# Optimization experiments

Measured on AMD Instinct MI355X. Metric: run time of the kernel, lower is better.

The kernel has to match this reference:

```python
import jax, jax.numpy as jnp
import numpy as np

N, E, IN, HID, OUT = 50000, 800000, 128, 64, 32
ALPHA, BETA, DIVIDER = 0.5, 0.5, 5.0


def _gcn_conv(x, edge_index, W, b, alpha=ALPHA, beta=BETA):
    """DirectedGCNConv.forward: add self loops, linear, degree-normalized gather-mul-scatter."""
    n = x.shape[0]
    loops = jnp.arange(n, dtype=edge_index.dtype)
    row = jnp.concatenate([edge_index[0], loops])  # sources
    col = jnp.concatenate([edge_index[1], loops])  # targets
    x = x @ W.T + b                                # [n, out]
    ones = jnp.ones(row.shape[0], dtype=x.dtype)
    in_deg = jax.ops.segment_sum(ones, col, num_segments=n)
    out_deg = jax.ops.segment_sum(ones, row, num_segments=n)
    norm = in_deg[col] ** (-alpha) * out_deg[row] ** (-beta)  # [E+n]
    msgs = norm[:, None] * x[row]                  # gather + scale
    return jax.ops.segment_sum(msgs, col, num_segments=n)  # scatter-add aggr


def _source_enc(x, ei, W1, b1, W2, b2):
    x = jax.nn.relu(_gcn_conv(x, ei, W1, b1))
    return _gcn_conv(x, jnp.flip(ei, axis=0), W2, b2)


def _target_enc(x, ei, W1, b1, W2, b2):
    x = jax.nn.relu(_gcn_conv(x, jnp.flip(ei, axis=0), W1, b1))
    return _gcn_conv(x, ei, W2, b2)


def setup_inputs() -> dict:
    key = jax.random.key(0)
    ks = jax.random.split(key, 24)

    def lin(kw, kb, o, i, scale):
        return (jax.random.normal(kw, (o, i), jnp.float32) * scale,
                jax.random.normal(kb, (o,), jnp.float32) * 0.01)

    s1 = (2.0 / (IN + HID)) ** 0.5
    s2 = (2.0 / (HID + OUT)) ** 0.5
    inp = {
        "s": jax.random.normal(ks[0], (N, IN), jnp.float32),
        "t": jax.random.normal(ks[1], (N, IN), jnp.float32),
        "edge_index": jax.random.randint(ks[2], (2, E), 0, N, jnp.int32),
        "noise_s": jax.random.normal(ks[3], (N, OUT), jnp.float32),
        "noise_t": jax.random.normal(ks[4], (N, OUT), jnp.float32),
    }
    names = ["sm", "sl", "tm", "tl"]  # source/target mu/logstd encoders
    k = 5
    for nm in names:
        W1, b1 = lin(ks[k], ks[k + 1], HID, IN, s1); k += 2
        W2, b2 = lin(ks[k], ks[k + 1], OUT, HID, s2); k += 2
        inp[nm + "1_W"], inp[nm + "1_b"] = W1, b1
        inp[nm + "2_W"], inp[nm + "2_b"] = W2, b2
    return inp


def reference(s, t, edge_index, noise_s, noise_t,
              sm1_W, sm1_b, sm2_W, sm2_b,
              sl1_W, sl1_b, sl2_W, sl2_b,
              tm1_W, tm1_b, tm2_W, tm2_b,
              tl1_W, tl1_b, tl2_W, tl2_b):
    s_mu = _source_enc(s, edge_index, sm1_W, sm1_b, sm2_W, sm2_b)
    s_logstd = _source_enc(s, edge_index, sl1_W, sl1_b, sl2_W, sl2_b)
    t_mu = _target_enc(t, edge_index, tm1_W, tm1_b, tm2_W, tm2_b)
    t_logstd = _target_enc(t, edge_index, tl1_W, tl1_b, tl2_W, tl2_b)
    # reparametrize_edges (training mode), noise materialized as input
    s_out = s_mu + noise_s * jnp.exp(s_logstd) / DIVIDER
    t_out = t_mu + noise_t * jnp.exp(t_logstd) / DIVIDER
    return (s_out, t_out)
```

## Files before the change

kernel.cpp:

```cpp
#include <hip/hip_runtime.h>
#include <hip/hip_fp16.h>
#include <math.h>

#define N_NODES 50000
#define NPACK 25000
#define E_EDGES 800000
#define NCHUNKS ((N_NODES + 1023) / 1024)
#define LIN_BLOCKS 1564
#define QCH 64
#define CHUNK (E_EDGES / QCH)
#define CHUNK4 (CHUNK / 4)
#define OCT_NODES 6250
#define OCT_PACK 3125
#define HF_BLOCKS 1024
#define FILL_GRID (HF_BLOCKS + LIN_BLOCKS)

typedef _Float16 half8 __attribute__((ext_vector_type(8)));
typedef float f32x4 __attribute__((ext_vector_type(4)));

__device__ inline float fac_from(unsigned int u) {
    unsigned short us = (unsigned short)(u >> 16);
    __half h;
    __builtin_memcpy(&h, &us, 2);
    return __half2float(h);
}

__device__ inline int unpack_cnt(const unsigned int* cntp, int i) {
    unsigned int w = cntp[i >> 1];
    return (i & 1) ? (int)(w >> 16) : (int)(w & 0xffff);
}

__device__ inline uint4 nt_load4(const uint4* p) {
    const unsigned long long* q = (const unsigned long long*)p;
    unsigned long long a = __builtin_nontemporal_load(q);
    unsigned long long b = __builtin_nontemporal_load(q + 1);
    uint4 r;
    r.x = (unsigned int)a; r.y = (unsigned int)(a >> 32);
    r.z = (unsigned int)b; r.w = (unsigned int)(b >> 32);
    return r;
}

__global__ __launch_bounds__(256) void hist_kernel(const int* __restrict__ ei0,
                                                   const int* __restrict__ ei1,
                                                   unsigned int* __restrict__ ghist) {
    __shared__ unsigned int h[OCT_PACK];
    int bx = blockIdx.x;
    int oct = bx & 7, q = (bx >> 3) & 63, dir = bx >> 9;
    int tid = threadIdx.x;
    for (int i = tid; i < OCT_PACK; i += 256) h[i] = 0;
    __syncthreads();
    const int* key = dir ? ei0 : ei1;
    const uint4* key4 = (const uint4*)(key + q * CHUNK);
    int lo = oct * OCT_NODES;
    for (int j = tid; j < CHUNK4; j += 256) {
        uint4 k4 = nt_load4(key4 + j);
        int vv[4] = { (int)k4.x, (int)k4.y, (int)k4.z, (int)k4.w };
#pragma unroll
        for (int e = 0; e < 4; ++e) {
            unsigned int d = (unsigned int)(vv[e] - lo);
            if (d < OCT_NODES) atomicAdd(&h[d >> 1], 1u << ((d & 1) * 16));
        }
    }
    __syncthreads();
    unsigned int* g = ghist + (size_t)(dir * QCH + q) * NPACK + oct * OCT_PACK;
    for (int i = tid; i < OCT_PACK; i += 256) g[i] = h[i];
}

__global__ __launch_bounds__(256) void nodescan_kernel(unsigned int* __restrict__ ghist,
                                                       unsigned int* __restrict__ cntp) {
    int vp = blockIdx.x * 256 + threadIdx.x;
    int dir = blockIdx.y;
    if (vp >= NPACK) return;
    unsigned int lo = 0, hi = 0;
    unsigned int* g = ghist + (size_t)dir * QCH * NPACK + vp;
#pragma unroll 4
    for (int q = 0; q < QCH; ++q) {
        unsigned int w = g[(size_t)q * NPACK];
        g[(size_t)q * NPACK] = lo | (hi << 16);
        lo += w & 0xffff;
        hi += w >> 16;
    }
    cntp[dir * NPACK + vp] = lo | (hi << 16);
}

__global__ __launch_bounds__(1024) void scan_chunk2_kernel(const unsigned int* __restrict__ cntp,
                                                           int* __restrict__ offs_f,
                                                           int* __restrict__ offs_b,
                                                           int* __restrict__ part_f,
                                                           int* __restrict__ part_b, int n) {
    const unsigned int* cnt = cntp + (blockIdx.y ? NPACK : 0);
    int* offs = blockIdx.y ? offs_b : offs_f;
    int* partials = blockIdx.y ? part_b : part_f;
    __shared__ int sh[1024];
    int tid = threadIdx.x;
    int i = blockIdx.x * 1024 + tid;
    int v = (i < n) ? unpack_cnt(cnt, i) : 0;
    sh[tid] = v;
    __syncthreads();
    for (int off = 1; off < 1024; off <<= 1) {
        int add = (tid >= off) ? sh[tid - off] : 0;
        __syncthreads();
        sh[tid] += add;
        __syncthreads();
    }
    if (i < n) offs[i] = sh[tid] - v;
    if (tid == 1023) partials[blockIdx.x] = sh[tid];
}

__global__ __launch_bounds__(64) void scan_partials2_kernel(int* part_f, int* part_b, int nchunks) {
    int* p = blockIdx.x ? part_b : part_f;
    __shared__ int sh[64];
    int tid = threadIdx.x;
    int v = (tid < nchunks) ? p[tid] : 0;
    sh[tid] = v;
    __syncthreads();
    for (int off = 1; off < 64; off <<= 1) {
        int add = (tid >= off) ? sh[tid - off] : 0;
        __syncthreads();
        sh[tid] += add;
        __syncthreads();
    }
    if (tid < nchunks) p[tid] = sh[tid] - v;
    if (tid == 63) p[nchunks] = sh[63];
}

__global__ __launch_bounds__(256) void addback_deg_kernel(int* __restrict__ offs_f,
                                                          int* __restrict__ offs_b,
                                                          const int* __restrict__ part_f,
                                                          const int* __restrict__ part_b,
                                                          const unsigned int* __restrict__ cntp,
                                                          float* dsi, float* dti,
                                                          unsigned short* __restrict__ h_dsi,
                                                          unsigned short* __restrict__ h_dti,
                                                          int n, int nchunks) {
    int i = blockIdx.x * 256 + threadIdx.x;
    if (blockIdx.y == 0) {
        if (i < n) {
            offs_f[i] += part_f[i >> 10];
            float f = rsqrtf((float)(unpack_cnt(cntp, i) + 1));
            dti[i] = f;
            __half hf = __float2half(f);
            unsigned short hb; __builtin_memcpy(&hb, &hf, 2);
            h_dti[i] = hb;
        } else if (i == n) offs_f[n] = part_f[nchunks];
    } else {
        if (i < n) {
            offs_b[i] += part_b[i >> 10];
            float f = rsqrtf((float)(unpack_cnt(cntp + NPACK, i) + 1));
            dsi[i] = f;
            __half hf = __float2half(f);
            unsigned short hb; __builtin_memcpy(&hb, &hf, 2);
            h_dsi[i] = hb;
        } else if (i == n) offs_b[n] = part_b[nchunks];
    }
}

__global__ __launch_bounds__(256) void fill_lin1_kernel(const int* __restrict__ ei0,
                                                        const int* __restrict__ ei1,
                                                        const unsigned int* __restrict__ ghist,
                                                        const int* __restrict__ offs_f,
                                                        const int* __restrict__ offs_b,
                                                        const unsigned short* __restrict__ h_dsi,
                                                        const unsigned short* __restrict__ h_dti,
                                                        unsigned int* __restrict__ pay_f,
                                                        unsigned int* __restrict__ pay_b,
                                                        const float* __restrict__ Xs,
                                                        const float* __restrict__ Xt,
                                                        const float* __restrict__ sWa,
                                                        const float* __restrict__ sba,
                                                        const float* __restrict__ sWb,
                                                        const float* __restrict__ sbb,
                                                        const float* __restrict__ tWa,
                                                        const float* __restrict__ tba,
                                                        const float* __restrict__ tWb,
                                                        const float* __restrict__ tbb,
                                                        __half* __restrict__ As,
                                                        __half* __restrict__ At, int n) {
    __shared__ unsigned int h[OCT_PACK];
    __shared__ unsigned int pref_sh[OCT_PACK];
    int bx = blockIdx.x;
    int tid = threadIdx.x;
    if (bx < HF_BLOCKS) {
        int oct = bx & 7, q = (bx >> 3) & 63, dir = bx >> 9;
        const unsigned int* pref = ghist + (size_t)(dir * QCH + q) * NPACK + oct * OCT_PACK;
        for (int i = tid; i < OCT_PACK; i += 256) {
            h[i] = 0;
            pref_sh[i] = __builtin_nontemporal_load(pref + i);
        }
        __syncthreads();
        const int* key = dir ? ei0 : ei1;
        const int* pid = dir ? ei1 : ei0;
        const unsigned short* hfac = dir ? h_dti : h_dsi;
        const int* offs = dir ? offs_b : offs_f;
        unsigned int* pay = dir ? pay_b : pay_f;
        const uint4* key4 = (const uint4*)(key + q * CHUNK);
        const uint4* pid4 = (const uint4*)(pid + q * CHUNK);
        int lo = oct * OCT_NODES;
        for (int j = tid; j < CHUNK4; j += 256) {
            uint4 k4 = nt_load4(key4 + j);
            uint4 p4 = nt_load4(pid4 + j);
            int vv[4] = { (int)k4.x, (int)k4.y, (int)k4.z, (int)k4.w };
            int pp[4] = { (int)p4.x, (int)p4.y, (int)p4.z, (int)p4.w };
#pragma unroll
            for (int e = 0; e < 4; ++e) {
                int v = vv[e];
                unsigned int d = (unsigned int)(v - lo);
                if (d < OCT_NODES) {
                    int sh = (d & 1) * 16;
                    unsigned int old = atomicAdd(&h[d >> 1], 1u << sh);
                    int rank = (int)((old >> sh) & 0xffff);
                    int cb = (int)((pref_sh[d >> 1] >> sh) & 0xffff);
                    int id = pp[e];
                    unsigned int hb = hfac[id];
                    pay[offs[v] + cb + rank] = (unsigned int)id | (hb << 16);
                }
            }
        }
        return;
    }
    int lidx = bx - HF_BLOCKS;
    int y = lidx & 1;
    int xb = lidx >> 1;
    const float* X = y ? Xt : Xs;
    const float* Wset[2] = { y ? tWa : sWa, y ? tWb : sWb };
    const float* bset[2] = { y ? tba : sba, y ? tbb : sbb };
    __half* A = y ? At : As;

    int w = tid >> 6, lane = tid & 63;
    int quad = lane >> 4, col = lane & 15;
    int node0 = xb * 64 + w * 16;

    half8 afrag[4];
    {
        int row = node0 + col;
        if (row >= n) row = n - 1;
        const float* xr = X + (size_t)row * 128 + quad * 8;
#pragma unroll
        for (int kc = 0; kc < 4; ++kc) {
            float4 f0 = *(const float4*)(xr + kc * 32);
            float4 f1 = *(const float4*)(xr + kc * 32 + 4);
            half8 hh;
            hh[0] = (_Float16)f0.x; hh[1] = (_Float16)f0.y;
            hh[2] = (_Float16)f0.z; hh[3] = (_Float16)f0.w;
            hh[4] = (_Float16)f1.x; hh[5] = (_Float16)f1.y;
            hh[6] = (_Float16)f1.z; hh[7] = (_Float16)f1.w;
            afrag[kc] = hh;
        }
    }

#pragma unroll
    for (int set = 0; set < 2; ++set) {
        const float* Ws = Wset[set];
#pragma unroll
        for (int nt = 0; nt < 4; ++nt) {
            float bb = bset[set][nt * 16 + col];
            f32x4 acc = { bb, bb, bb, bb };
            const float* wr = Ws + (size_t)(nt * 16 + col) * 128 + quad * 8;
#pragma unroll
            for (int kc = 0; kc < 4; ++kc) {
                float4 f0 = *(const float4*)(wr + kc * 32);
                float4 f1 = *(const float4*)(wr + kc * 32 + 4);
                half8 bfr;
                bfr[0] = (_Float16)f0.x; bfr[1] = (_Float16)f0.y;
                bfr[2] = (_Float16)f0.z; bfr[3] = (_Float16)f0.w;
                bfr[4] = (_Float16)f1.x; bfr[5] = (_Float16)f1.y;
                bfr[6] = (_Float16)f1.z; bfr[7] = (_Float16)f1.w;
                acc = __builtin_amdgcn_mfma_f32_16x16x32_f16(afrag[kc], bfr, acc, 0, 0, 0);
            }
#pragma unroll
            for (int r = 0; r < 4; ++r) {
                int node = node0 + quad * 4 + r;
                if (node < n)
                    A[(size_t)node * 128 + set * 64 + nt * 16 + col] = __float2half(acc[r]);
            }
        }
    }
}

__device__ inline void acc_fma(float* acc, uint4 u, float f) {
    const __half2* h = (const __half2*)&u;
    float2 f0 = __half22float2(h[0]);
    float2 f1 = __half22float2(h[1]);
    float2 f2 = __half22float2(h[2]);
    float2 f3 = __half22float2(h[3]);
    acc[0] += f * f0.x; acc[1] += f * f0.y; acc[2] += f * f1.x; acc[3] += f * f1.y;
    acc[4] += f * f2.x; acc[5] += f * f2.y; acc[6] += f * f3.x; acc[7] += f * f3.y;
}

__global__ __launch_bounds__(256) void pull_lin2_kernel(const __half* __restrict__ As,
                                                        const __half* __restrict__ At,
                                                        __half* __restrict__ Cs,
                                                        __half* __restrict__ Ct,
                                                        const int* __restrict__ offs_f,
                                                        const int* __restrict__ offs_b,
                                                        const unsigned int* __restrict__ pay_f,
                                                        const unsigned int* __restrict__ pay_b,
                                                        const float* __restrict__ dsi,
                                                        const float* __restrict__ dti,
                                                        const float* __restrict__ sW2a,
                                                        const float* __restrict__ sb2a,
                                                        const float* __restrict__ sW2b,
                                                        const float* __restrict__ sb2b,
                                                        const float* __restrict__ tW2a,
                                                        const float* __restrict__ tb2a,
                                                        const float* __restrict__ tW2b,
                                                        const float* __restrict__ tb2b, int n) {
    int y = blockIdx.y;
    const __half* xw = y ? At : As;
    __half* C = y ? Ct : Cs;
    const int* offs = y ? offs_b : offs_f;
    const unsigned int* pay = y ? pay_b : pay_f;
    const float* fac_self  = y ? dsi : dti;
    const float* fac_other = y ? dti : dsi;
    const float* W2a = y ? tW2a : sW2a;  const float* b2a = y ? tb2a : sb2a;
    const float* W2b = y ? tW2b : sW2b;  const float* b2b = y ? tb2b : sb2b;

    __shared__ float Wt[64 * 66];
    __shared__ float bsh[64];
    __shared__ float xs[16 * 132];

    int tid = threadIdx.x;
    for (int idx = tid; idx < 2048; idx += 256) {
        int o = idx >> 6, k = idx & 63;
        Wt[k * 66 + o]      = W2a[idx];
        Wt[k * 66 + 33 + o] = W2b[idx];
    }
    if (tid < 32) { bsh[tid] = b2a[tid]; bsh[32 + tid] = b2b[tid]; }

    int ln = tid >> 4;
    int f4 = tid & 15;
    int v = blockIdx.x * 16 + ln;
    int i = offs[v], end = offs[v + 1];
    const uint4* xw16 = (const uint4*)xw;

    float acc[8] = {0, 0, 0, 0, 0, 0, 0, 0};
    acc_fma(acc, xw16[v * 16 + f4], fac_other[v]);
    while (i < end && (i & 3)) {
        unsigned int pk = pay[i];
        acc_fma(acc, xw16[(pk & 0xffff) * 16 + f4], fac_from(pk));
        ++i;
    }
    for (; i + 3 < end; i += 4) {
        uint4 pk = *(const uint4*)(pay + i);
        int s0 = pk.x & 0xffff, s1 = pk.y & 0xffff;
        int s2 = pk.z & 0xffff, s3 = pk.w & 0xffff;
        uint4 ua = xw16[s0 * 16 + f4];
        uint4 ub = xw16[s1 * 16 + f4];
        uint4 uc = xw16[s2 * 16 + f4];
        uint4 ud = xw16[s3 * 16 + f4];
        acc_fma(acc, ua, fac_from(pk.x));
        acc_fma(acc, ub, fac_from(pk.y));
        acc_fma(acc, uc, fac_from(pk.z));
        acc_fma(acc, ud, fac_from(pk.w));
    }
    for (; i < end; ++i) {
        unsigned int pk = pay[i];
        acc_fma(acc, xw16[(pk & 0xffff) * 16 + f4], fac_from(pk));
    }

    float fs = fac_self[v];
    float4 a0, a1;
    a0.x = fmaxf(acc[0] * fs, 0.0f); a0.y = fmaxf(acc[1] * fs, 0.0f);
    a0.z = fmaxf(acc[2] * fs, 0.0f); a0.w = fmaxf(acc[3] * fs, 0.0f);
    a1.x = fmaxf(acc[4] * fs, 0.0f); a1.y = fmaxf(acc[5] * fs, 0.0f);
    a1.z = fmaxf(acc[6] * fs, 0.0f); a1.w = fmaxf(acc[7] * fs, 0.0f);
    *(float4*)&xs[ln * 132 + f4 * 8]     = a0;
    *(float4*)&xs[ln * 132 + f4 * 8 + 4] = a1;
    __syncthreads();

    int nn = tid >> 5, o = tid & 31;
    const float* x0 = &xs[nn * 132];
    const float* x1 = &xs[(nn + 8) * 132];
    float am0 = bsh[o], al0 = bsh[32 + o];
    float am1 = am0,    al1 = al0;
#pragma unroll 4
    for (int k = 0; k < 64; ++k) {
        float wm = Wt[k * 66 + o], wl = Wt[k * 66 + 33 + o];
        am0 += x0[k] * wm;  al0 += x0[64 + k] * wl;
        am1 += x1[k] * wm;  al1 += x1[64 + k] * wl;
    }
    int v0 = blockIdx.x * 16 + nn;
    int v1 = v0 + 8;
    C[v0 * 64 + o]      = __float2half(am0);
    C[v0 * 64 + 32 + o] = __float2half(al0);
    C[v1 * 64 + o]      = __float2half(am1);
    C[v1 * 64 + 32 + o] = __float2half(al1);
}

__global__ __launch_bounds__(256) void final_pull2_kernel(const __half* __restrict__ Cs,
                                                          const __half* __restrict__ Ct,
                                                          float* __restrict__ out_s,
                                                          float* __restrict__ out_t,
                                                          const int* __restrict__ offs_f,
                                                          const int* __restrict__ offs_b,
                                                          const unsigned int* __restrict__ pay_f,
                                                          const unsigned int* __restrict__ pay_b,
                                                          const float* __restrict__ dsi,
                                                          const float* __restrict__ dti,
                                                          const float* __restrict__ noise_s,
                                                          const float* __restrict__ noise_t,
                                                          int n) {
    int y = blockIdx.y;
    const __half* xw = y ? Ct : Cs;
    float* out = y ? out_t : out_s;
    const int* offs = y ? offs_f : offs_b;
    const unsigned int* pay = y ? pay_f : pay_b;
    const float* fac_self  = y ? dti : dsi;
    const float* fac_other = y ? dsi : dti;
    const float* noise = y ? noise_t : noise_s;

    const uint4* xw16 = (const uint4*)xw;
    int ln = threadIdx.x >> 3;
    int f4 = threadIdx.x & 7;
    int v = blockIdx.x * 32 + ln;
    if (v >= n) return;
    int i = offs[v], end = offs[v + 1];

    float acc[8] = {0, 0, 0, 0, 0, 0, 0, 0};
    acc_fma(acc, xw16[v * 8 + f4], fac_other[v]);
    while (i < end && (i & 3)) {
        unsigned int pk = pay[i];
        acc_fma(acc, xw16[(pk & 0xffff) * 8 + f4], fac_from(pk));
        ++i;
    }
    for (; i + 3 < end; i += 4) {
        uint4 pk = *(const uint4*)(pay + i);
        int s0 = pk.x & 0xffff, s1 = pk.y & 0xffff;
        int s2 = pk.z & 0xffff, s3 = pk.w & 0xffff;
        uint4 ua = xw16[s0 * 8 + f4];
        uint4 ub = xw16[s1 * 8 + f4];
        uint4 uc = xw16[s2 * 8 + f4];
        uint4 ud = xw16[s3 * 8 + f4];
        acc_fma(acc, ua, fac_from(pk.x));
        acc_fma(acc, ub, fac_from(pk.y));
        acc_fma(acc, uc, fac_from(pk.z));
        acc_fma(acc, ud, fac_from(pk.w));
    }
    for (; i < end; ++i) {
        unsigned int pk = pay[i];
        acc_fma(acc, xw16[(pk & 0xffff) * 8 + f4], fac_from(pk));
    }

    float fs = fac_self[v];
#pragma unroll
    for (int j = 0; j < 8; ++j) acc[j] *= fs;

    int lane = threadIdx.x & 63;
    float lg[8];
#pragma unroll
    for (int j = 0; j < 8; ++j) lg[j] = __shfl(acc[j], lane + 4);
    if (f4 < 4) {
        const float4* nz4 = (const float4*)noise;
        float4 n0 = nz4[v * 8 + f4 * 2];
        float4 n1 = nz4[v * 8 + f4 * 2 + 1];
        float4 r0, r1;
        r0.x = acc[0] + n0.x * expf(lg[0]) * 0.2f;
        r0.y = acc[1] + n0.y * expf(lg[1]) * 0.2f;
        r0.z = acc[2] + n0.z * expf(lg[2]) * 0.2f;
        r0.w = acc[3] + n0.w * expf(lg[3]) * 0.2f;
        r1.x = acc[4] + n1.x * expf(lg[4]) * 0.2f;
        r1.y = acc[5] + n1.y * expf(lg[5]) * 0.2f;
        r1.z = acc[6] + n1.z * expf(lg[6]) * 0.2f;
        r1.w = acc[7] + n1.w * expf(lg[7]) * 0.2f;
        float4* o4 = (float4*)out;
        o4[v * 8 + f4 * 2]     = r0;
        o4[v * 8 + f4 * 2 + 1] = r1;
    }
}

extern "C" void kernel_launch(void* const* d_in, const int* in_sizes, int n_in,
                              void* d_out, int out_size, void* d_ws, size_t ws_size,
                              hipStream_t stream) {
    const float* s       = (const float*)d_in[0];
    const float* t       = (const float*)d_in[1];
    const int*   ei      = (const int*)d_in[2];
    const float* noise_s = (const float*)d_in[3];
    const float* noise_t = (const float*)d_in[4];
    const float* sm1_W = (const float*)d_in[5];  const float* sm1_b = (const float*)d_in[6];
    const float* sm2_W = (const float*)d_in[7];  const float* sm2_b = (const float*)d_in[8];
    const float* sl1_W = (const float*)d_in[9];  const float* sl1_b = (const float*)d_in[10];
    const float* sl2_W = (const float*)d_in[11]; const float* sl2_b = (const float*)d_in[12];
    const float* tm1_W = (const float*)d_in[13]; const float* tm1_b = (const float*)d_in[14];
    const float* tm2_W = (const float*)d_in[15]; const float* tm2_b = (const float*)d_in[16];
    const float* tl1_W = (const float*)d_in[17]; const float* tl1_b = (const float*)d_in[18];
    const float* tl2_W = (const float*)d_in[19]; const float* tl2_b = (const float*)d_in[20];

    const int* ei0 = ei;
    const int* ei1 = ei + E_EDGES;

    __half* A_s = (__half*)d_ws;
    __half* A_t = A_s + (size_t)N_NODES * 128;
    __half* C_s = A_t + (size_t)N_NODES * 128;
    __half* C_t = C_s + (size_t)N_NODES * 64;
    unsigned int* pay_fwd = (unsigned int*)(C_t + (size_t)N_NODES * 64);
    unsigned int* pay_bwd = pay_fwd + E_EDGES;
    float* dsi = (float*)(pay_bwd + E_EDGES);
    float* dti = dsi + N_NODES;
    int* offs_fwd = (int*)(dti + N_NODES);
    int* offs_bwd = offs_fwd + N_NODES + 1;
    unsigned int* cntp = (unsigned int*)(offs_bwd + N_NODES + 1);
    int* part_fwd = (int*)(cntp + 2 * NPACK);
    int* part_bwd = part_fwd + NCHUNKS + 1;
    unsigned short* h_dsi = (unsigned short*)(part_bwd + NCHUNKS + 1);
    unsigned short* h_dti = h_dsi + N_NODES;

    unsigned int* ghist = (unsigned int*)C_s;

    float* s_out = (float*)d_out;
    float* t_out = (float*)d_out + N_NODES * 32;

    dim3 blk(256);
    dim3 agrid((N_NODES + 1 + 255) / 256, 2);
    dim3 pgrid(N_NODES / 16, 2);
    dim3 fgrid((N_NODES + 31) / 32, 2);
    dim3 nsgrid((NPACK + 255) / 256, 2);

    hist_kernel<<<HF_BLOCKS, blk, 0, stream>>>(ei0, ei1, ghist);
    nodescan_kernel<<<nsgrid, blk, 0, stream>>>(ghist, cntp);
    scan_chunk2_kernel<<<dim3(NCHUNKS, 2), 1024, 0, stream>>>(
        cntp, offs_fwd, offs_bwd, part_fwd, part_bwd, N_NODES);
    scan_partials2_kernel<<<2, 64, 0, stream>>>(part_fwd, part_bwd, NCHUNKS);
    addback_deg_kernel<<<agrid, blk, 0, stream>>>(offs_fwd, offs_bwd, part_fwd, part_bwd,
                                                  cntp, dsi, dti, h_dsi, h_dti,
                                                  N_NODES, NCHUNKS);
    fill_lin1_kernel<<<FILL_GRID, blk, 0, stream>>>(
        ei0, ei1, ghist, offs_fwd, offs_bwd, h_dsi, h_dti, pay_fwd, pay_bwd,
        s, t, sm1_W, sm1_b, sl1_W, sl1_b, tm1_W, tm1_b, tl1_W, tl1_b,
        A_s, A_t, N_NODES);

    pull_lin2_kernel<<<pgrid, blk, 0, stream>>>(A_s, A_t, C_s, C_t,
                                                offs_fwd, offs_bwd, pay_fwd, pay_bwd,
                                                dsi, dti,
                                                sm2_W, sm2_b, sl2_W, sl2_b,
                                                tm2_W, tm2_b, tl2_W, tl2_b, N_NODES);
    final_pull2_kernel<<<fgrid, blk, 0, stream>>>(C_s, C_t, s_out, t_out,
                                                  offs_fwd, offs_bwd, pay_fwd, pay_bwd,
                                                  dsi, dti, noise_s, noise_t, N_NODES);
}
```

Before: 369.2 us.

## Record per-bucket edge lists in histogram pass; fill only listed edges

The histogram pass now also writes, for each (direction, chunk, node-range) bucket, a compact list of edge indices that fall in that range, using wave ballot plus a shared counter. The fill kernel then reads only those listed edges, instead of rescanning the whole key chunk in all eight range blocks. Output positions come from per-node shared cursors built from prefix offsets. The first linear layer moves from the fill kernel into the histogram kernel's extra blocks. The lists are capped at a fixed capacity, so a bucket that overflows would silently drop edges, and edge order within a node becomes nondeterministic.

```diff
diff --git a/kernel.cpp b/kernel.cpp
--- a/kernel.cpp
+++ b/kernel.cpp
@@ -13,7 +13,8 @@
 #define OCT_NODES 6250
 #define OCT_PACK 3125
 #define HF_BLOCKS 1024
-#define FILL_GRID (HF_BLOCKS + LIN_BLOCKS)
+#define HL_GRID (HF_BLOCKS + LIN_BLOCKS)
+#define LCAP 2048
 
 typedef _Float16 half8 __attribute__((ext_vector_type(8)));
 typedef float f32x4 __attribute__((ext_vector_type(4)));
@@ -30,40 +31,121 @@
     return (i & 1) ? (int)(w >> 16) : (int)(w & 0xffff);
 }
 
-__device__ inline uint4 nt_load4(const uint4* p) {
-    const unsigned long long* q = (const unsigned long long*)p;
-    unsigned long long a = __builtin_nontemporal_load(q);
-    unsigned long long b = __builtin_nontemporal_load(q + 1);
-    uint4 r;
-    r.x = (unsigned int)a; r.y = (unsigned int)(a >> 32);
-    r.z = (unsigned int)b; r.w = (unsigned int)(b >> 32);
-    return r;
-}
-
-__global__ __launch_bounds__(256) void hist_kernel(const int* __restrict__ ei0,
-                                                   const int* __restrict__ ei1,
-                                                   unsigned int* __restrict__ ghist) {
+__global__ __launch_bounds__(256) void hist_lin1_kernel(const int* __restrict__ ei0,
+                                                        const int* __restrict__ ei1,
+                                                        unsigned int* __restrict__ ghist,
+                                                        unsigned short* __restrict__ list,
+                                                        unsigned int* __restrict__ cnt_bkt,
+                                                        const float* __restrict__ Xs,
+                                                        const float* __restrict__ Xt,
+                                                        const float* __restrict__ sWa,
+                                                        const float* __restrict__ sba,
+                                                        const float* __restrict__ sWb,
+                                                        const float* __restrict__ sbb,
+                                                        const float* __restrict__ tWa,
+                                                        const float* __restrict__ tba,
+                                                        const float* __restrict__ tWb,
+                                                        const float* __restrict__ tbb,
+                                                        __half* __restrict__ As,
+                                                        __half* __restrict__ At, int n) {
     __shared__ unsigned int h[OCT_PACK];
+    __shared__ unsigned int lcnt;
     int bx = blockIdx.x;
-    int oct = bx & 7, q = (bx >> 3) & 63, dir = bx >> 9;
     int tid = threadIdx.x;
-    for (int i = tid; i < OCT_PACK; i += 256) h[i] = 0;
-    __syncthreads();
-    const int* key = dir ? ei0 : ei1;
-    const uint4* key4 = (const uint4*)(key + q * CHUNK);
-    int lo = oct * OCT_NODES;
-    for (int j = tid; j < CHUNK4; j += 256) {
-        uint4 k4 = nt_load4(key4 + j);
-        int vv[4] = { (int)k4.x, (int)k4.y, (int)k4.z, (int)k4.w };
-#pragma unroll
-        for (int e = 0; e < 4; ++e) {
-            unsigned int d = (unsigned int)(vv[e] - lo);
-            if (d < OCT_NODES) atomicAdd(&h[d >> 1], 1u << ((d & 1) * 16));
+    if (bx < HF_BLOCKS) {
+        int oct = bx & 7, q = (bx >> 3) & 63, dir = bx >> 9;
+        for (int i = tid; i < OCT_PACK; i += 256) h[i] = 0;
+        if (tid == 0) lcnt = 0;
+        __syncthreads();
+        const int* key = dir ? ei0 : ei1;
+        const uint4* key4 = (const uint4*)(key + q * CHUNK);
+        unsigned short* lst = list + ((size_t)(dir * QCH + q) * 8 + oct) * LCAP;
+        int lo = oct * OCT_NODES;
+        int lane = tid & 63;
+        for (int j = tid; j < CHUNK4; j += 256) {
+            uint4 k4 = key4[j];
+            int vv[4] = { (int)k4.x, (int)k4.y, (int)k4.z, (int)k4.w };
+#pragma unroll
+            for (int e = 0; e < 4; ++e) {
+                unsigned int d = (unsigned int)(vv[e] - lo);
+                bool pred = d < OCT_NODES;
+                if (pred) atomicAdd(&h[d >> 1], 1u << ((d & 1) * 16));
+                unsigned long long m = __ballot(pred);
+                if (m) {
+                    int pre = __popcll(m & ((1ull << lane) - 1));
+                    int tot = __popcll(m);
+                    int ldr = __ffsll((unsigned long long)m) - 1;
+                    unsigned int base = 0;
+                    if (lane == ldr) base = atomicAdd(&lcnt, (unsigned int)tot);
+                    base = __shfl(base, ldr);
+                    unsigned int slot = base + (unsigned int)pre;
+                    if (pred && slot < LCAP) lst[slot] = (unsigned short)(j * 4 + e);
+                }
+            }
         }
-    }
-    __syncthreads();
-    unsigned int* g = ghist + (size_t)(dir * QCH + q) * NPACK + oct * OCT_PACK;
-    for (int i = tid; i < OCT_PACK; i += 256) g[i] = h[i];
+        __syncthreads();
+        unsigned int* g = ghist + (size_t)(dir * QCH + q) * NPACK + oct * OCT_PACK;
+        for (int i = tid; i < OCT_PACK; i += 256) g[i] = h[i];
+        if (tid == 0) cnt_bkt[dir * 512 + q * 8 + oct] = (lcnt < LCAP) ? lcnt : LCAP;
+        return;
+    }
+    int lidx = bx - HF_BLOCKS;
+    int y = lidx & 1;
+    int xb = lidx >> 1;
+    const float* X = y ? Xt : Xs;
+    const float* Wset[2] = { y ? tWa : sWa, y ? tWb : sWb };
+    const float* bset[2] = { y ? tba : sba, y ? tbb : sbb };
+    __half* A = y ? At : As;
+
+    int w = tid >> 6, lane = tid & 63;
+    int quad = lane >> 4, col = lane & 15;
+    int node0 = xb * 64 + w * 16;
+
+    half8 afrag[4];
+    {
+        int row = node0 + col;
+        if (row >= n) row = n - 1;
+        const float* xr = X + (size_t)row * 128 + quad * 8;
+#pragma unroll
+        for (int kc = 0; kc < 4; ++kc) {
+            float4 f0 = *(const float4*)(xr + kc * 32);
+            float4 f1 = *(const float4*)(xr + kc * 32 + 4);
+            half8 hh;
+            hh[0] = (_Float16)f0.x; hh[1] = (_Float16)f0.y;
+            hh[2] = (_Float16)f0.z; hh[3] = (_Float16)f0.w;
+            hh[4] = (_Float16)f1.x; hh[5] = (_Float16)f1.y;
+            hh[6] = (_Float16)f1.z; hh[7] = (_Float16)f1.w;
+            afrag[kc] = hh;
+        }
+    }
+
+#pragma unroll
+    for (int set = 0; set < 2; ++set) {
+        const float* Ws = Wset[set];
+#pragma unroll
+        for (int nt = 0; nt < 4; ++nt) {
+            float bb = bset[set][nt * 16 + col];
+            f32x4 acc = { bb, bb, bb, bb };
+            const float* wr = Ws + (size_t)(nt * 16 + col) * 128 + quad * 8;
+#pragma unroll
+            for (int kc = 0; kc < 4; ++kc) {
+                float4 f0 = *(const float4*)(wr + kc * 32);
+                float4 f1 = *(const float4*)(wr + kc * 32 + 4);
+                half8 bfr;
+                bfr[0] = (_Float16)f0.x; bfr[1] = (_Float16)f0.y;
+                bfr[2] = (_Float16)f0.z; bfr[3] = (_Float16)f0.w;
+                bfr[4] = (_Float16)f1.x; bfr[5] = (_Float16)f1.y;
+                bfr[6] = (_Float16)f1.z; bfr[7] = (_Float16)f1.w;
+                acc = __builtin_amdgcn_mfma_f32_16x16x32_f16(afrag[kc], bfr, acc, 0, 0, 0);
+            }
+#pragma unroll
+            for (int r = 0; r < 4; ++r) {
+                int node = node0 + quad * 4 + r;
+                if (node < n)
+                    A[(size_t)node * 128 + set * 64 + nt * 16 + col] = __float2half(acc[r]);
+            }
+        }
+    }
 }
 
 __global__ __launch_bounds__(256) void nodescan_kernel(unsigned int* __restrict__ ghist,
@@ -155,125 +237,44 @@
     }
 }
 
-__global__ __launch_bounds__(256) void fill_lin1_kernel(const int* __restrict__ ei0,
-                                                        const int* __restrict__ ei1,
-                                                        const unsigned int* __restrict__ ghist,
-                                                        const int* __restrict__ offs_f,
-                                                        const int* __restrict__ offs_b,
-                                                        const unsigned short* __restrict__ h_dsi,
-                                                        const unsigned short* __restrict__ h_dti,
-                                                        unsigned int* __restrict__ pay_f,
-                                                        unsigned int* __restrict__ pay_b,
-                                                        const float* __restrict__ Xs,
-                                                        const float* __restrict__ Xt,
-                                                        const float* __restrict__ sWa,
-                                                        const float* __restrict__ sba,
-                                                        const float* __restrict__ sWb,
-                                                        const float* __restrict__ sbb,
-                                                        const float* __restrict__ tWa,
-                                                        const float* __restrict__ tba,
-                                                        const float* __restrict__ tWb,
-                                                        const float* __restrict__ tbb,
-                                                        __half* __restrict__ As,
-                                                        __half* __restrict__ At, int n) {
-    __shared__ unsigned int h[OCT_PACK];
-    __shared__ unsigned int pref_sh[OCT_PACK];
+__global__ __launch_bounds__(256) void fill_kernel(const int* __restrict__ ei0,
+                                                   const int* __restrict__ ei1,
+                                                   const unsigned int* __restrict__ ghist,
+                                                   const int* __restrict__ offs_f,
+                                                   const int* __restrict__ offs_b,
+                                                   const unsigned short* __restrict__ h_dsi,
+                                                   const unsigned short* __restrict__ h_dti,
+                                                   unsigned int* __restrict__ pay_f,
+                                                   unsigned int* __restrict__ pay_b,
+                                                   const unsigned short* __restrict__ list,
+                                                   const unsigned int* __restrict__ cnt_bkt) {
+    __shared__ unsigned int pos[OCT_NODES];
     int bx = blockIdx.x;
+    int oct = bx & 7, q = (bx >> 3) & 63, dir = bx >> 9;
     int tid = threadIdx.x;
-    if (bx < HF_BLOCKS) {
-        int oct = bx & 7, q = (bx >> 3) & 63, dir = bx >> 9;
-        const unsigned int* pref = ghist + (size_t)(dir * QCH + q) * NPACK + oct * OCT_PACK;
-        for (int i = tid; i < OCT_PACK; i += 256) {
-            h[i] = 0;
-            pref_sh[i] = __builtin_nontemporal_load(pref + i);
-        }
-        __syncthreads();
-        const int* key = dir ? ei0 : ei1;
-        const int* pid = dir ? ei1 : ei0;
-        const unsigned short* hfac = dir ? h_dti : h_dsi;
-        const int* offs = dir ? offs_b : offs_f;
-        unsigned int* pay = dir ? pay_b : pay_f;
-        const uint4* key4 = (const uint4*)(key + q * CHUNK);
-        const uint4* pid4 = (const uint4*)(pid + q * CHUNK);
-        int lo = oct * OCT_NODES;
-        for (int j = tid; j < CHUNK4; j += 256) {
-            uint4 k4 = nt_load4(key4 + j);
-            uint4 p4 = nt_load4(pid4 + j);
-            int vv[4] = { (int)k4.x, (int)k4.y, (int)k4.z, (int)k4.w };
-            int pp[4] = { (int)p4.x, (int)p4.y, (int)p4.z, (int)p4.w };
-#pragma unroll
-            for (int e = 0; e < 4; ++e) {
-                int v = vv[e];
-                unsigned int d = (unsigned int)(v - lo);
-                if (d < OCT_NODES) {
-                    int sh = (d & 1) * 16;
-                    unsigned int old = atomicAdd(&h[d >> 1], 1u << sh);
-                    int rank = (int)((old >> sh) & 0xffff);
-                    int cb = (int)((pref_sh[d >> 1] >> sh) & 0xffff);
-                    int id = pp[e];
-                    unsigned int hb = hfac[id];
-                    pay[offs[v] + cb + rank] = (unsigned int)id | (hb << 16);
-                }
-            }
-        }
-        return;
-    }
-    int lidx = bx - HF_BLOCKS;
-    int y = lidx & 1;
-    int xb = lidx >> 1;
-    const float* X = y ? Xt : Xs;
-    const float* Wset[2] = { y ? tWa : sWa, y ? tWb : sWb };
-    const float* bset[2] = { y ? tba : sba, y ? tbb : sbb };
-    __half* A = y ? At : As;
-
-    int w = tid >> 6, lane = tid & 63;
-    int quad = lane >> 4, col = lane & 15;
-    int node0 = xb * 64 + w * 16;
-
-    half8 afrag[4];
-    {
-        int row = node0 + col;
-        if (row >= n) row = n - 1;
-        const float* xr = X + (size_t)row * 128 + quad * 8;
-#pragma unroll
-        for (int kc = 0; kc < 4; ++kc) {
-            float4 f0 = *(const float4*)(xr + kc * 32);
-            float4 f1 = *(const float4*)(xr + kc * 32 + 4);
-            half8 hh;
-            hh[0] = (_Float16)f0.x; hh[1] = (_Float16)f0.y;
-            hh[2] = (_Float16)f0.z; hh[3] = (_Float16)f0.w;
-            hh[4] = (_Float16)f1.x; hh[5] = (_Float16)f1.y;
-            hh[6] = (_Float16)f1.z; hh[7] = (_Float16)f1.w;
-            afrag[kc] = hh;
-        }
-    }
-
-#pragma unroll
-    for (int set = 0; set < 2; ++set) {
-        const float* Ws = Wset[set];
-#pragma unroll
-        for (int nt = 0; nt < 4; ++nt) {
-            float bb = bset[set][nt * 16 + col];
-            f32x4 acc = { bb, bb, bb, bb };
-            const float* wr = Ws + (size_t)(nt * 16 + col) * 128 + quad * 8;
-#pragma unroll
-            for (int kc = 0; kc < 4; ++kc) {
-                float4 f0 = *(const float4*)(wr + kc * 32);
-                float4 f1 = *(const float4*)(wr + kc * 32 + 4);
-                half8 bfr;
-                bfr[0] = (_Float16)f0.x; bfr[1] = (_Float16)f0.y;
-                bfr[2] = (_Float16)f0.z; bfr[3] = (_Float16)f0.w;
-                bfr[4] = (_Float16)f1.x; bfr[5] = (_Float16)f1.y;
-                bfr[6] = (_Float16)f1.z; bfr[7] = (_Float16)f1.w;
-                acc = __builtin_amdgcn_mfma_f32_16x16x32_f16(afrag[kc], bfr, acc, 0, 0, 0);
-            }
-#pragma unroll
-            for (int r = 0; r < 4; ++r) {
-                int node = node0 + quad * 4 + r;
-                if (node < n)
-                    A[(size_t)node * 128 + set * 64 + nt * 16 + col] = __float2half(acc[r]);
-            }
-        }
+    const unsigned int* pref = ghist + (size_t)(dir * QCH + q) * NPACK + oct * OCT_PACK;
+    const int* offs = dir ? offs_b : offs_f;
+    int lo = oct * OCT_NODES;
+    for (int d = tid; d < OCT_NODES; d += 256) {
+        unsigned int pw = pref[d >> 1];
+        int cb = (d & 1) ? (int)(pw >> 16) : (int)(pw & 0xffff);
+        pos[d] = (unsigned int)(offs[lo + d] + cb);
+    }
+    __syncthreads();
+    const int* key = dir ? ei0 : ei1;
+    const int* pid = dir ? ei1 : ei0;
+    const unsigned short* hfac = dir ? h_dti : h_dsi;
+    unsigned int* pay = dir ? pay_b : pay_f;
+    const unsigned short* lst = list + ((size_t)(dir * QCH + q) * 8 + oct) * LCAP;
+    int cnt = (int)cnt_bkt[dir * 512 + q * 8 + oct];
+    int base = q * CHUNK;
+    for (int j = tid; j < cnt; j += 256) {
+        int gi = base + (int)lst[j];
+        int v = key[gi];
+        int id = pid[gi];
+        unsigned int p = atomicAdd(&pos[v - lo], 1u);
+        unsigned int hb = hfac[id];
+        pay[p] = (unsigned int)id | (hb << 16);
     }
 }
 
@@ -503,6 +504,8 @@
     int* part_bwd = part_fwd + NCHUNKS + 1;
     unsigned short* h_dsi = (unsigned short*)(part_bwd + NCHUNKS + 1);
     unsigned short* h_dti = h_dsi + N_NODES;
+    unsigned short* list  = h_dti + N_NODES;
+    unsigned int* cnt_bkt = (unsigned int*)(list + (size_t)HF_BLOCKS * LCAP);
 
     unsigned int* ghist = (unsigned int*)C_s;
 
@@ -515,7 +518,10 @@
     dim3 fgrid((N_NODES + 31) / 32, 2);
     dim3 nsgrid((NPACK + 255) / 256, 2);
 
-    hist_kernel<<<HF_BLOCKS, blk, 0, stream>>>(ei0, ei1, ghist);
+    hist_lin1_kernel<<<HL_GRID, blk, 0, stream>>>(
+        ei0, ei1, ghist, list, cnt_bkt,
+        s, t, sm1_W, sm1_b, sl1_W, sl1_b, tm1_W, tm1_b, tl1_W, tl1_b,
+        A_s, A_t, N_NODES);
     nodescan_kernel<<<nsgrid, blk, 0, stream>>>(ghist, cntp);
     scan_chunk2_kernel<<<dim3(NCHUNKS, 2), 1024, 0, stream>>>(
         cntp, offs_fwd, offs_bwd, part_fwd, part_bwd, N_NODES);
@@ -523,10 +529,9 @@
     addback_deg_kernel<<<agrid, blk, 0, stream>>>(offs_fwd, offs_bwd, part_fwd, part_bwd,
                                                   cntp, dsi, dti, h_dsi, h_dti,
                                                   N_NODES, NCHUNKS);
-    fill_lin1_kernel<<<FILL_GRID, blk, 0, stream>>>(
-        ei0, ei1, ghist, offs_fwd, offs_bwd, h_dsi, h_dti, pay_fwd, pay_bwd,
-        s, t, sm1_W, sm1_b, sl1_W, sl1_b, tm1_W, tm1_b, tl1_W, tl1_b,
-        A_s, A_t, N_NODES);
+    fill_kernel<<<HF_BLOCKS, blk, 0, stream>>>(ei0, ei1, ghist, offs_fwd, offs_bwd,
+                                               h_dsi, h_dti, pay_fwd, pay_bwd,
+                                               list, cnt_bkt);
 
     pull_lin2_kernel<<<pgrid, blk, 0, stream>>>(A_s, A_t, C_s, C_t,
                                                 offs_fwd, offs_bwd, pay_fwd, pay_bwd,
```

Result: faster. 337.1 us (-8.7%).
